# Kernel tuning notes

Measured on AMD Instinct MI355X. Metric: run time of the kernel, lower is better.

## Reference

```python
import jax, jax.numpy as jnp
import numpy as np

BN_EPS = 1e-5
N_HEADS = 8


def _mha_kv1(q_in, kv, Wqkv, bqkv, Wo, bo):
    # torch.nn.MultiheadAttention (batch_first) with a length-1 key/value.
    B, L, C = q_in.shape
    hd = C // N_HEADS
    Wq, Wk, Wv = Wqkv[:C], Wqkv[C:2 * C], Wqkv[2 * C:]
    bq, bk, bv = bqkv[:C], bqkv[C:2 * C], bqkv[2 * C:]
    q = (q_in @ Wq.T + bq).reshape(B, L, N_HEADS, hd)
    k = (kv @ Wk.T + bk).reshape(B, 1, N_HEADS, hd)
    v = (kv @ Wv.T + bv).reshape(B, 1, N_HEADS, hd)
    scores = jnp.einsum('blhd,bmhd->bhlm', q, k) / jnp.sqrt(jnp.asarray(hd, q.dtype))
    attn = jax.nn.softmax(scores, axis=-1)  # kv len = 1 -> all ones
    out = jnp.einsum('bhlm,bmhd->blhd', attn, v).reshape(B, L, C)
    return out @ Wo.T + bo


def setup_inputs() -> dict:
    key = jax.random.key(0)
    ks = jax.random.split(key, 16)
    B, C, H, W = 8, 512, 64, 64
    Td = 512
    s = 0.02
    return {
        'rgb_c4': jax.random.normal(ks[0], (B, C, H, W), jnp.float32),
        'depth_c4': jax.random.normal(ks[1], (B, C, H, W), jnp.float32),
        'text_feat': jax.random.normal(ks[2], (B, Td), jnp.float32),
        'tp_w': jax.random.normal(ks[3], (C, Td), jnp.float32) * s,
        'tp_b': jnp.zeros((C,), jnp.float32),
        'rgb_wqkv': jax.random.normal(ks[4], (3 * C, C), jnp.float32) * s,
        'rgb_bqkv': jnp.zeros((3 * C,), jnp.float32),
        'rgb_wo': jax.random.normal(ks[5], (C, C), jnp.float32) * s,
        'rgb_bo': jnp.zeros((C,), jnp.float32),
        'dep_wqkv': jax.random.normal(ks[6], (3 * C, C), jnp.float32) * s,
        'dep_bqkv': jnp.zeros((3 * C,), jnp.float32),
        'dep_wo': jax.random.normal(ks[7], (C, C), jnp.float32) * s,
        'dep_bo': jnp.zeros((C,), jnp.float32),
        'gate_w': jax.random.normal(ks[8], (C, 2 * C), jnp.float32) * s,  # 1x1 conv kernel squeezed
        'gate_b': jnp.zeros((C,), jnp.float32),
        'bn_g': jnp.ones((C,), jnp.float32),
        'bn_b': jnp.zeros((C,), jnp.float32),
    }


def reference(rgb_c4, depth_c4, text_feat, tp_w, tp_b,
              rgb_wqkv, rgb_bqkv, rgb_wo, rgb_bo,
              dep_wqkv, dep_bqkv, dep_wo, dep_bo,
              gate_w, gate_b, bn_g, bn_b):
    B, C, H, W = rgb_c4.shape
    text_proj = text_feat @ tp_w.T + tp_b            # (B, C)
    kv = text_proj[:, None, :]                        # (B, 1, C)

    rgb_flat = rgb_c4.reshape(B, C, H * W).transpose(0, 2, 1)   # (B, HW, C)
    dep_flat = depth_c4.reshape(B, C, H * W).transpose(0, 2, 1)
    rgb_t = _mha_kv1(rgb_flat, kv, rgb_wqkv, rgb_bqkv, rgb_wo, rgb_bo)
    dep_t = _mha_kv1(dep_flat, kv, dep_wqkv, dep_bqkv, dep_wo, dep_bo)
    rgb_t = rgb_t.transpose(0, 2, 1).reshape(B, C, H, W)
    dep_t = dep_t.transpose(0, 2, 1).reshape(B, C, H, W)

    gate_in = jnp.concatenate([rgb_t, dep_t], axis=1)           # (B, 2C, H, W)
    pre = jnp.einsum('bihw,oi->bohw', gate_in, gate_w) + gate_b[None, :, None, None]
    mean = pre.mean(axis=(0, 2, 3))
    var = pre.var(axis=(0, 2, 3))                               # biased var (BN training mode)
    xhat = (pre - mean[None, :, None, None]) * jax.lax.rsqrt(var + BN_EPS)[None, :, None, None]
    gate = jax.nn.sigmoid(bn_g[None, :, None, None] * xhat + bn_b[None, :, None, None])

    fused = gate * rgb_t + (1.0 - gate) * dep_t
    pixel_loss = jnp.mean((rgb_c4 - depth_c4) ** 2)
    depth_loss = jnp.mean(jnp.abs(depth_c4 - jax.lax.stop_gradient(rgb_c4)))
    return fused, pixel_loss, depth_loss
```

## Files before the change

### kernel.cpp

```cpp
#include <hip/hip_runtime.h>
#include <hip/hip_bf16.h>
#include <math.h>


#define BB 8
#define CC 512
#define TOTAL (8 * 512 * 4096)
#define N4 (TOTAL / 4)
#define Q4 (N4 / 4)
#define CHAINB 128
#define LOSSB_A 896
#define LOSSB_B 512
#define NPART 3200

typedef float f32x4 __attribute__((ext_vector_type(4)));

__device__ __forceinline__ void mv8(
    const float* __restrict__ Wrow, const float* __restrict__ x, int ldx,
    int K, int lane, float* acc)
{
    #pragma unroll
    for (int b = 0; b < BB; ++b) acc[b] = 0.0f;
    const f32x4* W4 = (const f32x4*)Wrow;
    const int K4 = K >> 2;
    for (int t = lane; t < K4; t += 64) {
        f32x4 w = W4[t];
        #pragma unroll
        for (int b = 0; b < BB; ++b) {
            f32x4 xv = ((const f32x4*)(x + b * ldx))[t];
            acc[b] += w.x * xv.x + w.y * xv.y + w.z * xv.z + w.w * xv.w;
        }
    }
    #pragma unroll
    for (int off = 32; off > 0; off >>= 1) {
        #pragma unroll
        for (int b = 0; b < BB; ++b)
            acc[b] += __shfl_xor(acc[b], off, 64);
    }
}

__device__ __forceinline__ void loss_chunk(
    const f32x4* __restrict__ rgb, const f32x4* __restrict__ dep,
    int start, int nblocks, int lid, float* __restrict__ partials, int pidx)
{
    const int stride = nblocks * 256;
    float ssq = 0.0f, sab = 0.0f;
    for (int j = start + lid * 256 + threadIdx.x; j < start + Q4; j += stride) {
        f32x4 a = __builtin_nontemporal_load(&rgb[j]);
        f32x4 b = __builtin_nontemporal_load(&dep[j]);
        float d0 = a.x - b.x, d1 = a.y - b.y, d2 = a.z - b.z, d3 = a.w - b.w;
        ssq += d0 * d0 + d1 * d1 + d2 * d2 + d3 * d3;
        sab += fabsf(d0) + fabsf(d1) + fabsf(d2) + fabsf(d3);
    }
    #pragma unroll
    for (int off = 32; off > 0; off >>= 1) {
        ssq += __shfl_xor(ssq, off, 64);
        sab += __shfl_xor(sab, off, 64);
    }
    __shared__ float ls[8];
    const int lane = threadIdx.x & 63;
    const int wv   = threadIdx.x >> 6;
    if (lane == 0) { ls[wv] = ssq; ls[4 + wv] = sab; }
    __syncthreads();
    if (threadIdx.x == 0) {
        partials[pidx]         = ls[0] + ls[1] + ls[2] + ls[3];
        partials[4096 + pidx]  = ls[4] + ls[5] + ls[6] + ls[7];
    }
}

__global__ __launch_bounds__(256) void k_stage(
    int stage,
    const float* __restrict__ text,
    const float* __restrict__ tp_w,  const float* __restrict__ tp_b,
    const float* __restrict__ rwqkv, const float* __restrict__ rbqkv,
    const float* __restrict__ dwqkv, const float* __restrict__ dbqkv,
    const float* __restrict__ rwo,   const float* __restrict__ rbo,
    const float* __restrict__ dwo,   const float* __restrict__ dbo,
    float* __restrict__ tp, float* __restrict__ vr, float* __restrict__ vd,
    float* __restrict__ rd,
    const f32x4* __restrict__ rgb, const f32x4* __restrict__ dep,
    float* __restrict__ partials)
{
    const int lane = threadIdx.x & 63;
    if (blockIdx.x < CHAINB) {
        const int w = (blockIdx.x << 2) + (threadIdx.x >> 6);
        float acc[BB];
        if (stage == 1) {
            mv8(tp_w + (size_t)w * 512, text, 512, 512, lane, acc);
            if (lane == 0) {
                float bs = tp_b[w];
                #pragma unroll
                for (int b = 0; b < BB; ++b) tp[b * 512 + w] = acc[b] + bs;
            }
        } else if (stage == 2) {
            mv8(rwqkv + (size_t)(1024 + w) * 512, tp, 512, 512, lane, acc);
            if (lane == 0) {
                float bs = rbqkv[1024 + w];
                #pragma unroll
                for (int b = 0; b < BB; ++b) vr[b * 512 + w] = acc[b] + bs;
            }
            mv8(dwqkv + (size_t)(1024 + w) * 512, tp, 512, 512, lane, acc);
            if (lane == 0) {
                float bs = dbqkv[1024 + w];
                #pragma unroll
                for (int b = 0; b < BB; ++b) vd[b * 512 + w] = acc[b] + bs;
            }
        } else {
            mv8(rwo + (size_t)w * 512, vr, 512, 512, lane, acc);
            if (lane == 0) {
                float bs = rbo[w];
                #pragma unroll
                for (int b = 0; b < BB; ++b) rd[b * 1024 + w] = acc[b] + bs;
            }
            mv8(dwo + (size_t)w * 512, vd, 512, 512, lane, acc);
            if (lane == 0) {
                float bs = dbo[w];
                #pragma unroll
                for (int b = 0; b < BB; ++b) rd[b * 1024 + 512 + w] = acc[b] + bs;
            }
        }
    } else {
        const int chunk = stage - 1;
        const int lid   = blockIdx.x - CHAINB;
        loss_chunk(rgb, dep, chunk * Q4, LOSSB_A, lid, partials,
                   chunk * LOSSB_A + lid);
    }
}

__global__ __launch_bounds__(256) void k_gate_bcast(
    const float* __restrict__ gw,  const float* __restrict__ gb,
    const float* __restrict__ rd,
    const float* __restrict__ bng, const float* __restrict__ bnb,
    const f32x4* __restrict__ rgb, const f32x4* __restrict__ dep,
    f32x4* __restrict__ out, float* __restrict__ partials)
{
    const int lane = threadIdx.x & 63;
    if (blockIdx.x < 512) {
        const int g = blockIdx.x & 127;
        const int q = blockIdx.x >> 7;
        const int o = (g << 2) + (threadIdx.x >> 6);
        float acc[BB];
        mv8(gw + (size_t)o * 1024, rd, 1024, 1024, lane, acc);
        float bsv = gb[o];
        float pre[BB];
        float mean = 0.0f;
        #pragma unroll
        for (int b = 0; b < BB; ++b) { pre[b] = acc[b] + bsv; mean += pre[b]; }
        mean *= 0.125f;
        float var = 0.0f;
        #pragma unroll
        for (int b = 0; b < BB; ++b) { float dv = pre[b] - mean; var += dv * dv; }
        var *= 0.125f;
        float inv = rsqrtf(var + 1e-5f);
        float gg = bng[o], bb2 = bnb[o];
        #pragma unroll
        for (int b = 0; b < BB; ++b) {
            float xh = (pre[b] - mean) * inv;
            float z  = gg * xh + bb2;
            float gt = 1.0f / (1.0f + expf(-z));
            float rv = rd[b * 1024 + o];
            float dv = rd[b * 1024 + 512 + o];
            float f  = gt * rv + (1.0f - gt) * dv;
            f32x4 v  = {f, f, f, f};
            const int base = b * 524288 + o * 1024 + q * 256;
            #pragma unroll
            for (int i = 0; i < 4; ++i)
                __builtin_nontemporal_store(v, &out[base + i * 64 + lane]);
        }
    } else {
        const int lid = blockIdx.x - 512;
        loss_chunk(rgb, dep, 3 * Q4, LOSSB_B, lid, partials,
                   3 * LOSSB_A + lid);
    }
}

__global__ __launch_bounds__(256) void k_final(
    const float* __restrict__ partials, float* __restrict__ out_sc)
{
    float ssq = 0.0f, sab = 0.0f;
    for (int i = threadIdx.x; i < NPART; i += 256) {
        ssq += partials[i];
        sab += partials[4096 + i];
    }
    #pragma unroll
    for (int off = 32; off > 0; off >>= 1) {
        ssq += __shfl_xor(ssq, off, 64);
        sab += __shfl_xor(sab, off, 64);
    }
    __shared__ float ls[8];
    const int lane = threadIdx.x & 63;
    const int wv   = threadIdx.x >> 6;
    if (lane == 0) { ls[wv] = ssq; ls[4 + wv] = sab; }
    __syncthreads();
    if (threadIdx.x == 0) {
        const float invN = 1.0f / (float)TOTAL;
        out_sc[0] = (ls[0] + ls[1] + ls[2] + ls[3]) * invN;
        out_sc[1] = (ls[4] + ls[5] + ls[6] + ls[7]) * invN;
    }
}

extern "C" void kernel_launch(void* const* d_in, const int* in_sizes, int n_in,
                              void* d_out, int out_size, void* d_ws, size_t ws_size,
                              hipStream_t stream) {
    const float* rgb   = (const float*)d_in[0];
    const float* dep   = (const float*)d_in[1];
    const float* text  = (const float*)d_in[2];
    const float* tp_w  = (const float*)d_in[3];
    const float* tp_b  = (const float*)d_in[4];
    const float* rwqkv = (const float*)d_in[5];
    const float* rbqkv = (const float*)d_in[6];
    const float* rwo   = (const float*)d_in[7];
    const float* rbo   = (const float*)d_in[8];
    const float* dwqkv = (const float*)d_in[9];
    const float* dbqkv = (const float*)d_in[10];
    const float* dwo   = (const float*)d_in[11];
    const float* dbo   = (const float*)d_in[12];
    const float* gw    = (const float*)d_in[13];
    const float* gb    = (const float*)d_in[14];
    const float* bng   = (const float*)d_in[15];
    const float* bnb   = (const float*)d_in[16];

    float* ws  = (float*)d_ws;
    float* tp  = ws;
    float* vr  = ws + 4096;
    float* vd  = ws + 8192;
    float* rd  = ws + 12288;
    float* partials = ws + 20480;

    float* outf   = (float*)d_out;
    float* out_sc = outf + TOTAL;

    const f32x4* rgb4 = (const f32x4*)rgb;
    const f32x4* dep4 = (const f32x4*)dep;

    for (int stage = 1; stage <= 3; ++stage) {
        k_stage<<<CHAINB + LOSSB_A, 256, 0, stream>>>(
            stage, text, tp_w, tp_b, rwqkv, rbqkv, dwqkv, dbqkv,
            rwo, rbo, dwo, dbo, tp, vr, vd, rd, rgb4, dep4, partials);
    }

    k_gate_bcast<<<512 + LOSSB_B, 256, 0, stream>>>(
        gw, gb, rd, bng, bnb, rgb4, dep4, (f32x4*)outf, partials);

    k_final<<<1, 256, 0, stream>>>(partials, out_sc);
}
```

Baseline: 213.0 us.

## Collapse matvec chain into per-batch blocks in one kernel alongside loss reduction

Replaces the three staged launches plus the gate and final kernels with two launches. One block per batch element runs the whole text-projection, V-projection, output-projection and gate-conv matvec chain with intermediates kept in LDS, while the other blocks compute the full loss reduction concurrently. The final loss reduction moves into an extra block of the broadcast kernel. This removes several launch boundaries and the serial stage dependencies. In exchange each chain block now streams all the weights by itself, so only 8 blocks carry the serial chain, and that could become the critical path.

```diff
diff --git a/kernel.cpp b/kernel.cpp
--- a/kernel.cpp
+++ b/kernel.cpp
@@ -1,5 +1,4 @@
 #include <hip/hip_runtime.h>
-#include <hip/hip_bf16.h>
 #include <math.h>
 
 
@@ -7,155 +6,134 @@
 #define CC 512
 #define TOTAL (8 * 512 * 4096)
 #define N4 (TOTAL / 4)
-#define Q4 (N4 / 4)
-#define CHAINB 128
-#define LOSSB_A 896
-#define LOSSB_B 512
-#define NPART 3200
+#define LOSSA 1016
+#define NP LOSSA
 
 typedef float f32x4 __attribute__((ext_vector_type(4)));
 
-__device__ __forceinline__ void mv8(
-    const float* __restrict__ Wrow, const float* __restrict__ x, int ldx,
-    int K, int lane, float* acc)
+__device__ __forceinline__ float wave_dot(const float* __restrict__ Wrow,
+                                          const float* xlds, int K4, int lane)
 {
-    #pragma unroll
-    for (int b = 0; b < BB; ++b) acc[b] = 0.0f;
     const f32x4* W4 = (const f32x4*)Wrow;
-    const int K4 = K >> 2;
+    const f32x4* x4 = (const f32x4*)xlds;
+    float s = 0.0f;
     for (int t = lane; t < K4; t += 64) {
         f32x4 w = W4[t];
-        #pragma unroll
-        for (int b = 0; b < BB; ++b) {
-            f32x4 xv = ((const f32x4*)(x + b * ldx))[t];
-            acc[b] += w.x * xv.x + w.y * xv.y + w.z * xv.z + w.w * xv.w;
-        }
+        f32x4 x = x4[t];
+        s += w.x * x.x + w.y * x.y + w.z * x.z + w.w * x.w;
     }
     #pragma unroll
-    for (int off = 32; off > 0; off >>= 1) {
-        #pragma unroll
-        for (int b = 0; b < BB; ++b)
-            acc[b] += __shfl_xor(acc[b], off, 64);
-    }
-}
-
-__device__ __forceinline__ void loss_chunk(
-    const f32x4* __restrict__ rgb, const f32x4* __restrict__ dep,
-    int start, int nblocks, int lid, float* __restrict__ partials, int pidx)
-{
-    const int stride = nblocks * 256;
-    float ssq = 0.0f, sab = 0.0f;
-    for (int j = start + lid * 256 + threadIdx.x; j < start + Q4; j += stride) {
-        f32x4 a = __builtin_nontemporal_load(&rgb[j]);
-        f32x4 b = __builtin_nontemporal_load(&dep[j]);
-        float d0 = a.x - b.x, d1 = a.y - b.y, d2 = a.z - b.z, d3 = a.w - b.w;
-        ssq += d0 * d0 + d1 * d1 + d2 * d2 + d3 * d3;
-        sab += fabsf(d0) + fabsf(d1) + fabsf(d2) + fabsf(d3);
-    }
-    #pragma unroll
-    for (int off = 32; off > 0; off >>= 1) {
-        ssq += __shfl_xor(ssq, off, 64);
-        sab += __shfl_xor(sab, off, 64);
-    }
-    __shared__ float ls[8];
-    const int lane = threadIdx.x & 63;
-    const int wv   = threadIdx.x >> 6;
-    if (lane == 0) { ls[wv] = ssq; ls[4 + wv] = sab; }
-    __syncthreads();
-    if (threadIdx.x == 0) {
-        partials[pidx]         = ls[0] + ls[1] + ls[2] + ls[3];
-        partials[4096 + pidx]  = ls[4] + ls[5] + ls[6] + ls[7];
-    }
-}
-
-__global__ __launch_bounds__(256) void k_stage(
-    int stage,
+    for (int off = 32; off > 0; off >>= 1)
+        s += __shfl_xor(s, off, 64);
+    return s;
+}
+
+__global__ __launch_bounds__(512) void k_chain_loss(
     const float* __restrict__ text,
     const float* __restrict__ tp_w,  const float* __restrict__ tp_b,
     const float* __restrict__ rwqkv, const float* __restrict__ rbqkv,
     const float* __restrict__ dwqkv, const float* __restrict__ dbqkv,
     const float* __restrict__ rwo,   const float* __restrict__ rbo,
     const float* __restrict__ dwo,   const float* __restrict__ dbo,
-    float* __restrict__ tp, float* __restrict__ vr, float* __restrict__ vd,
-    float* __restrict__ rd,
+    const float* __restrict__ gw,    const float* __restrict__ gb,
+    float* __restrict__ pre, float* __restrict__ rd,
     const f32x4* __restrict__ rgb, const f32x4* __restrict__ dep,
     float* __restrict__ partials)
 {
     const int lane = threadIdx.x & 63;
-    if (blockIdx.x < CHAINB) {
-        const int w = (blockIdx.x << 2) + (threadIdx.x >> 6);
-        float acc[BB];
-        if (stage == 1) {
-            mv8(tp_w + (size_t)w * 512, text, 512, 512, lane, acc);
+    const int wv   = threadIdx.x >> 6;
+    if (blockIdx.x < BB) {
+        __shared__ float bufA[1024];
+        __shared__ float bufB[1024];
+        const int b = blockIdx.x;
+        if (threadIdx.x < 512)
+            bufA[threadIdx.x] = text[b * 512 + threadIdx.x];
+        __syncthreads();
+        for (int i = 0; i < 64; ++i) {
+            const int o = (wv << 6) + i;
+            float s = wave_dot(tp_w + (size_t)o * 512, bufA, 128, lane) + tp_b[o];
+            if (lane == 0) bufB[o] = s;
+        }
+        __syncthreads();
+        for (int i = 0; i < 64; ++i) {
+            const int o = (wv << 6) + i;
+            float sr = wave_dot(rwqkv + (size_t)(1024 + o) * 512, bufB, 128, lane)
+                       + rbqkv[1024 + o];
+            float sd = wave_dot(dwqkv + (size_t)(1024 + o) * 512, bufB, 128, lane)
+                       + dbqkv[1024 + o];
+            if (lane == 0) { bufA[o] = sr; bufA[512 + o] = sd; }
+        }
+        __syncthreads();
+        for (int i = 0; i < 64; ++i) {
+            const int o = (wv << 6) + i;
+            float sr = wave_dot(rwo + (size_t)o * 512, bufA, 128, lane) + rbo[o];
+            float sd = wave_dot(dwo + (size_t)o * 512, bufA + 512, 128, lane) + dbo[o];
             if (lane == 0) {
-                float bs = tp_b[w];
-                #pragma unroll
-                for (int b = 0; b < BB; ++b) tp[b * 512 + w] = acc[b] + bs;
+                bufB[o] = sr; bufB[512 + o] = sd;
+                rd[b * 1024 + o] = sr; rd[b * 1024 + 512 + o] = sd;
             }
-        } else if (stage == 2) {
-            mv8(rwqkv + (size_t)(1024 + w) * 512, tp, 512, 512, lane, acc);
-            if (lane == 0) {
-                float bs = rbqkv[1024 + w];
-                #pragma unroll
-                for (int b = 0; b < BB; ++b) vr[b * 512 + w] = acc[b] + bs;
-            }
-            mv8(dwqkv + (size_t)(1024 + w) * 512, tp, 512, 512, lane, acc);
-            if (lane == 0) {
-                float bs = dbqkv[1024 + w];
-                #pragma unroll
-                for (int b = 0; b < BB; ++b) vd[b * 512 + w] = acc[b] + bs;
-            }
-        } else {
-            mv8(rwo + (size_t)w * 512, vr, 512, 512, lane, acc);
-            if (lane == 0) {
-                float bs = rbo[w];
-                #pragma unroll
-                for (int b = 0; b < BB; ++b) rd[b * 1024 + w] = acc[b] + bs;
-            }
-            mv8(dwo + (size_t)w * 512, vd, 512, 512, lane, acc);
-            if (lane == 0) {
-                float bs = dbo[w];
-                #pragma unroll
-                for (int b = 0; b < BB; ++b) rd[b * 1024 + 512 + w] = acc[b] + bs;
-            }
+        }
+        __syncthreads();
+        for (int i = 0; i < 64; ++i) {
+            const int o = (wv << 6) + i;
+            float s = wave_dot(gw + (size_t)o * 1024, bufB, 256, lane) + gb[o];
+            if (lane == 0) pre[b * 512 + o] = s;
         }
     } else {
-        const int chunk = stage - 1;
-        const int lid   = blockIdx.x - CHAINB;
-        loss_chunk(rgb, dep, chunk * Q4, LOSSB_A, lid, partials,
-                   chunk * LOSSB_A + lid);
+        const int lid = blockIdx.x - BB;
+        float ssq = 0.0f, sab = 0.0f;
+        const int stride = LOSSA * 512;
+        for (int j = lid * 512 + threadIdx.x; j < N4; j += stride) {
+            f32x4 a  = __builtin_nontemporal_load(&rgb[j]);
+            f32x4 b2 = __builtin_nontemporal_load(&dep[j]);
+            float d0 = a.x - b2.x, d1 = a.y - b2.y;
+            float d2 = a.z - b2.z, d3 = a.w - b2.w;
+            ssq += d0 * d0 + d1 * d1 + d2 * d2 + d3 * d3;
+            sab += fabsf(d0) + fabsf(d1) + fabsf(d2) + fabsf(d3);
+        }
+        #pragma unroll
+        for (int off = 32; off > 0; off >>= 1) {
+            ssq += __shfl_xor(ssq, off, 64);
+            sab += __shfl_xor(sab, off, 64);
+        }
+        __shared__ float ls[16];
+        if (lane == 0) { ls[wv] = ssq; ls[8 + wv] = sab; }
+        __syncthreads();
+        if (threadIdx.x == 0) {
+            float a = 0.0f, c = 0.0f;
+            #pragma unroll
+            for (int k = 0; k < 8; ++k) { a += ls[k]; c += ls[8 + k]; }
+            partials[lid] = a;
+            partials[2048 + lid] = c;
+        }
     }
 }
 
-__global__ __launch_bounds__(256) void k_gate_bcast(
-    const float* __restrict__ gw,  const float* __restrict__ gb,
-    const float* __restrict__ rd,
+__global__ __launch_bounds__(256) void k_bcast_final(
+    const float* __restrict__ pre, const float* __restrict__ rd,
     const float* __restrict__ bng, const float* __restrict__ bnb,
-    const f32x4* __restrict__ rgb, const f32x4* __restrict__ dep,
-    f32x4* __restrict__ out, float* __restrict__ partials)
+    f32x4* __restrict__ out, const float* __restrict__ partials,
+    float* __restrict__ out_sc)
 {
     const int lane = threadIdx.x & 63;
     if (blockIdx.x < 512) {
         const int g = blockIdx.x & 127;
         const int q = blockIdx.x >> 7;
         const int o = (g << 2) + (threadIdx.x >> 6);
-        float acc[BB];
-        mv8(gw + (size_t)o * 1024, rd, 1024, 1024, lane, acc);
-        float bsv = gb[o];
-        float pre[BB];
+        float pr[BB];
         float mean = 0.0f;
         #pragma unroll
-        for (int b = 0; b < BB; ++b) { pre[b] = acc[b] + bsv; mean += pre[b]; }
+        for (int b = 0; b < BB; ++b) { pr[b] = pre[b * 512 + o]; mean += pr[b]; }
         mean *= 0.125f;
         float var = 0.0f;
         #pragma unroll
-        for (int b = 0; b < BB; ++b) { float dv = pre[b] - mean; var += dv * dv; }
+        for (int b = 0; b < BB; ++b) { float dv = pr[b] - mean; var += dv * dv; }
         var *= 0.125f;
         float inv = rsqrtf(var + 1e-5f);
         float gg = bng[o], bb2 = bnb[o];
         #pragma unroll
         for (int b = 0; b < BB; ++b) {
-            float xh = (pre[b] - mean) * inv;
+            float xh = (pr[b] - mean) * inv;
             float z  = gg * xh + bb2;
             float gt = 1.0f / (1.0f + expf(-z));
             float rv = rd[b * 1024 + o];
@@ -168,34 +146,25 @@
                 __builtin_nontemporal_store(v, &out[base + i * 64 + lane]);
         }
     } else {
-        const int lid = blockIdx.x - 512;
-        loss_chunk(rgb, dep, 3 * Q4, LOSSB_B, lid, partials,
-                   3 * LOSSB_A + lid);
-    }
-}
-
-__global__ __launch_bounds__(256) void k_final(
-    const float* __restrict__ partials, float* __restrict__ out_sc)
-{
-    float ssq = 0.0f, sab = 0.0f;
-    for (int i = threadIdx.x; i < NPART; i += 256) {
-        ssq += partials[i];
-        sab += partials[4096 + i];
-    }
-    #pragma unroll
-    for (int off = 32; off > 0; off >>= 1) {
-        ssq += __shfl_xor(ssq, off, 64);
-        sab += __shfl_xor(sab, off, 64);
-    }
-    __shared__ float ls[8];
-    const int lane = threadIdx.x & 63;
-    const int wv   = threadIdx.x >> 6;
-    if (lane == 0) { ls[wv] = ssq; ls[4 + wv] = sab; }
-    __syncthreads();
-    if (threadIdx.x == 0) {
-        const float invN = 1.0f / (float)TOTAL;
-        out_sc[0] = (ls[0] + ls[1] + ls[2] + ls[3]) * invN;
-        out_sc[1] = (ls[4] + ls[5] + ls[6] + ls[7]) * invN;
+        float ssq = 0.0f, sab = 0.0f;
+        for (int i = threadIdx.x; i < NP; i += 256) {
+            ssq += partials[i];
+            sab += partials[2048 + i];
+        }
+        #pragma unroll
+        for (int off = 32; off > 0; off >>= 1) {
+            ssq += __shfl_xor(ssq, off, 64);
+            sab += __shfl_xor(sab, off, 64);
+        }
+        __shared__ float ls[8];
+        const int wv = threadIdx.x >> 6;
+        if (lane == 0) { ls[wv] = ssq; ls[4 + wv] = sab; }
+        __syncthreads();
+        if (threadIdx.x == 0) {
+            const float invN = 1.0f / (float)TOTAL;
+            out_sc[0] = (ls[0] + ls[1] + ls[2] + ls[3]) * invN;
+            out_sc[1] = (ls[4] + ls[5] + ls[6] + ls[7]) * invN;
+        }
     }
 }
 
@@ -221,11 +190,9 @@
     const float* bnb   = (const float*)d_in[16];
 
     float* ws  = (float*)d_ws;
-    float* tp  = ws;
-    float* vr  = ws + 4096;
-    float* vd  = ws + 8192;
-    float* rd  = ws + 12288;
-    float* partials = ws + 20480;
+    float* pre = ws;
+    float* rd  = ws + 4096;
+    float* partials = ws + 12288;
 
     float* outf   = (float*)d_out;
     float* out_sc = outf + TOTAL;
@@ -233,14 +200,10 @@
     const f32x4* rgb4 = (const f32x4*)rgb;
     const f32x4* dep4 = (const f32x4*)dep;
 
-    for (int stage = 1; stage <= 3; ++stage) {
-        k_stage<<<CHAINB + LOSSB_A, 256, 0, stream>>>(
-            stage, text, tp_w, tp_b, rwqkv, rbqkv, dwqkv, dbqkv,
-            rwo, rbo, dwo, dbo, tp, vr, vd, rd, rgb4, dep4, partials);
-    }
-
-    k_gate_bcast<<<512 + LOSSB_B, 256, 0, stream>>>(
-        gw, gb, rd, bng, bnb, rgb4, dep4, (f32x4*)outf, partials);
-
-    k_final<<<1, 256, 0, stream>>>(partials, out_sc);
-}
+    k_chain_loss<<<BB + LOSSA, 512, 0, stream>>>(
+        text, tp_w, tp_b, rwqkv, rbqkv, dwqkv, dbqkv,
+        rwo, rbo, dwo, dbo, gw, gb, pre, rd, rgb4, dep4, partials);
+
+    k_bcast_final<<<512 + 1, 256, 0, stream>>>(
+        pre, rd, bng, bnb, (f32x4*)outf, partials, out_sc);
+}
```

New measurement: 597.3 us. 180% more time.

## Split loss reduction over three chain stages and fold final reduce into gate kernel

Applied to the files above, without the earlier changes.

The loss streaming work, previously split into four quarters with the last quarter overlapped with the gate/broadcast kernel, is now split into three thirds handled alongside the three chain stages. The gate kernel no longer streams rgb/depth, so it can do its broadcast writes without competing for bandwidth. The final partial-sum reduction runs in one extra block of the gate kernel, which removes a separate launch. Each chain stage now carries more loss traffic, which could lengthen those stages if the chain work was not the critical path.

```diff
diff --git a/kernel.cpp b/kernel.cpp
--- a/kernel.cpp
+++ b/kernel.cpp
@@ -1,5 +1,4 @@
 #include <hip/hip_runtime.h>
-#include <hip/hip_bf16.h>
 #include <math.h>
 
 
@@ -7,11 +6,11 @@
 #define CC 512
 #define TOTAL (8 * 512 * 4096)
 #define N4 (TOTAL / 4)
-#define Q4 (N4 / 4)
+#define T1 1398102
+#define T2 2796203
 #define CHAINB 128
 #define LOSSB_A 896
-#define LOSSB_B 512
-#define NPART 3200
+#define NPART (3 * LOSSB_A)
 
 typedef float f32x4 __attribute__((ext_vector_type(4)));
 
@@ -41,11 +40,12 @@
 
 __device__ __forceinline__ void loss_chunk(
     const f32x4* __restrict__ rgb, const f32x4* __restrict__ dep,
-    int start, int nblocks, int lid, float* __restrict__ partials, int pidx)
+    int start, int end, int nblocks, int lid, float* __restrict__ partials,
+    int pidx)
 {
     const int stride = nblocks * 256;
     float ssq = 0.0f, sab = 0.0f;
-    for (int j = start + lid * 256 + threadIdx.x; j < start + Q4; j += stride) {
+    for (int j = start + lid * 256 + threadIdx.x; j < end; j += stride) {
         f32x4 a = __builtin_nontemporal_load(&rgb[j]);
         f32x4 b = __builtin_nontemporal_load(&dep[j]);
         float d0 = a.x - b.x, d1 = a.y - b.y, d2 = a.z - b.z, d3 = a.w - b.w;
@@ -122,7 +122,9 @@
     } else {
         const int chunk = stage - 1;
         const int lid   = blockIdx.x - CHAINB;
-        loss_chunk(rgb, dep, chunk * Q4, LOSSB_A, lid, partials,
+        const int s0 = (chunk == 0) ? 0  : (chunk == 1) ? T1 : T2;
+        const int e0 = (chunk == 0) ? T1 : (chunk == 1) ? T2 : N4;
+        loss_chunk(rgb, dep, s0, e0, LOSSB_A, lid, partials,
                    chunk * LOSSB_A + lid);
     }
 }
@@ -131,8 +133,8 @@
     const float* __restrict__ gw,  const float* __restrict__ gb,
     const float* __restrict__ rd,
     const float* __restrict__ bng, const float* __restrict__ bnb,
-    const f32x4* __restrict__ rgb, const f32x4* __restrict__ dep,
-    f32x4* __restrict__ out, float* __restrict__ partials)
+    f32x4* __restrict__ out, const float* __restrict__ partials,
+    float* __restrict__ out_sc)
 {
     const int lane = threadIdx.x & 63;
     if (blockIdx.x < 512) {
@@ -168,34 +170,25 @@
                 __builtin_nontemporal_store(v, &out[base + i * 64 + lane]);
         }
     } else {
-        const int lid = blockIdx.x - 512;
-        loss_chunk(rgb, dep, 3 * Q4, LOSSB_B, lid, partials,
-                   3 * LOSSB_A + lid);
-    }
-}
-
-__global__ __launch_bounds__(256) void k_final(
-    const float* __restrict__ partials, float* __restrict__ out_sc)
-{
-    float ssq = 0.0f, sab = 0.0f;
-    for (int i = threadIdx.x; i < NPART; i += 256) {
-        ssq += partials[i];
-        sab += partials[4096 + i];
-    }
-    #pragma unroll
-    for (int off = 32; off > 0; off >>= 1) {
-        ssq += __shfl_xor(ssq, off, 64);
-        sab += __shfl_xor(sab, off, 64);
-    }
-    __shared__ float ls[8];
-    const int lane = threadIdx.x & 63;
-    const int wv   = threadIdx.x >> 6;
-    if (lane == 0) { ls[wv] = ssq; ls[4 + wv] = sab; }
-    __syncthreads();
-    if (threadIdx.x == 0) {
-        const float invN = 1.0f / (float)TOTAL;
-        out_sc[0] = (ls[0] + ls[1] + ls[2] + ls[3]) * invN;
-        out_sc[1] = (ls[4] + ls[5] + ls[6] + ls[7]) * invN;
+        float ssq = 0.0f, sab = 0.0f;
+        for (int i = threadIdx.x; i < NPART; i += 256) {
+            ssq += partials[i];
+            sab += partials[4096 + i];
+        }
+        #pragma unroll
+        for (int off = 32; off > 0; off >>= 1) {
+            ssq += __shfl_xor(ssq, off, 64);
+            sab += __shfl_xor(sab, off, 64);
+        }
+        __shared__ float ls[8];
+        const int wv = threadIdx.x >> 6;
+        if (lane == 0) { ls[wv] = ssq; ls[4 + wv] = sab; }
+        __syncthreads();
+        if (threadIdx.x == 0) {
+            const float invN = 1.0f / (float)TOTAL;
+            out_sc[0] = (ls[0] + ls[1] + ls[2] + ls[3]) * invN;
+            out_sc[1] = (ls[4] + ls[5] + ls[6] + ls[7]) * invN;
+        }
     }
 }
 
@@ -239,8 +232,6 @@
             rwo, rbo, dwo, dbo, tp, vr, vd, rd, rgb4, dep4, partials);
     }
 
-    k_gate_bcast<<<512 + LOSSB_B, 256, 0, stream>>>(
-        gw, gb, rd, bng, bnb, rgb4, dep4, (f32x4*)outf, partials);
-
-    k_final<<<1, 256, 0, stream>>>(partials, out_sc);
-}
+    k_gate_bcast<<<512 + 1, 256, 0, stream>>>(
+        gw, gb, rd, bng, bnb, (f32x4*)outf, partials, out_sc);
+}
```

New measurement: 204.6 us. 1.04x faster.
